# Performance work log

Measured on AMD Instinct MI355X. Metric: run time of the kernel, lower is better.

## Reference

```python
import jax, jax.numpy as jnp
import numpy as np

DIM = 320
D_STATE = 32
D_CONV = 4
EXPAND = 2
HEADDIM = 80
D_INNER = EXPAND * DIM          # 640
NHEADS = D_INNER // HEADDIM     # 8
NGROUPS = 1
CONV_DIM = D_INNER + 2 * NGROUPS * D_STATE          # 704
D_IN_PROJ = 2 * D_INNER + 2 * NGROUPS * D_STATE + NHEADS  # 1352
PATCH = (16, 16, 16)
NUM_PT_EMB = 2


def setup_inputs() -> dict:
    key = jax.random.key(0)
    ks = jax.random.split(key, 16)
    B, Np = 4, 8
    x = jax.random.normal(ks[0], (B, DIM) + PATCH, dtype=jnp.float32)
    point_coords = jax.random.uniform(ks[1], (B, Np, 3), dtype=jnp.float32) * jnp.asarray(PATCH, jnp.float32)
    point_labels = jax.random.randint(ks[2], (B, Np), 0, 2)
    return {
        "x": x,
        "point_coords": point_coords,
        "ln_w": jnp.ones((DIM,), jnp.float32),
        "ln_b": jnp.zeros((DIM,), jnp.float32),
        "in_proj_w": jax.random.normal(ks[3], (D_IN_PROJ, DIM), jnp.float32) * 0.02,
        "conv_w": jax.random.normal(ks[4], (CONV_DIM, 1, D_CONV), jnp.float32) * 0.2,
        "conv_b": jax.random.normal(ks[5], (CONV_DIM,), jnp.float32) * 0.02,
        "dt_bias": jax.random.uniform(ks[6], (NHEADS,), jnp.float32, 0.0, 0.1),
        "A_log": jnp.log(jax.random.uniform(ks[7], (NHEADS,), jnp.float32, 1.0, 16.0)),
        "Dp": jnp.ones((NHEADS,), jnp.float32),
        "rms_w": jnp.ones((D_INNER,), jnp.float32),
        "out_proj_w": jax.random.normal(ks[8], (DIM, D_INNER), jnp.float32) * 0.02,
        "pe_gauss": jax.random.normal(ks[9], (3, DIM // 2), jnp.float32),
        "point_embed": jax.random.normal(ks[10], (NUM_PT_EMB, DIM), jnp.float32) * 0.02,
        "not_a_point": jax.random.normal(ks[11], (DIM,), jnp.float32) * 0.02,
        "point_labels": point_labels,
    }


def _forward(x, point_coords, ln_w, ln_b, in_proj_w, conv_w, conv_b, dt_bias,
             A_log, Dp, rms_w, out_proj_w, pe_gauss, point_embed, not_a_point,
             point_labels):
    B, C = x.shape[:2]
    img_dims = x.shape[2:]
    n_tokens = int(np.prod(img_dims))
    xf = x.reshape(B, C, n_tokens).transpose(0, 2, 1)  # (B, T, C)

    # ---- PointEncoder (SAM-style random Fourier positional embedding) ----
    pc = point_coords / jnp.asarray(PATCH, x.dtype)     # normalize to [0,1]
    pc = 2.0 * pc - 1.0
    pe = (2.0 * jnp.pi) * (pc @ pe_gauss)               # (B, Np, DIM/2)
    pemb = jnp.concatenate([jnp.sin(pe), jnp.cos(pe)], axis=-1)  # (B, Np, DIM)
    lbl = point_labels[..., None]
    safe = jnp.clip(point_labels, 0, NUM_PT_EMB - 1)
    pemb = jnp.where(lbl == -1, not_a_point, pemb + point_embed[safe])

    seq = jnp.concatenate([xf, pemb], axis=1)           # (B, L, C)
    L = seq.shape[1]

    # ---- LayerNorm ----
    mu = seq.mean(-1, keepdims=True)
    var = jnp.mean((seq - mu) ** 2, axis=-1, keepdims=True)
    xn = (seq - mu) * jax.lax.rsqrt(var + 1e-5) * ln_w + ln_b

    # ---- Mamba2 ----
    zxbcdt = xn @ in_proj_w.T                            # (B, L, 1352)
    z = zxbcdt[..., :D_INNER]
    xBC = zxbcdt[..., D_INNER:D_INNER + CONV_DIM]
    dt = zxbcdt[..., D_INNER + CONV_DIM:]                # (B, L, H)
    dt = jax.nn.softplus(dt + dt_bias)

    # causal depthwise conv1d over channels
    conv = jax.lax.conv_general_dilated(
        xBC.transpose(0, 2, 1), conv_w, (1,), [(D_CONV - 1, 0)],
        feature_group_count=CONV_DIM,
        dimension_numbers=("NCH", "OIH", "NCH"))
    xBC = jax.nn.silu((conv + conv_b[None, :, None]).transpose(0, 2, 1))

    xs = xBC[..., :D_INNER].reshape(B, L, NHEADS, HEADDIM)
    Bm = xBC[..., D_INNER:D_INNER + D_STATE]             # (B, L, N), ngroups=1
    Cm = xBC[..., D_INNER + D_STATE:]                    # (B, L, N)

    A = -jnp.exp(A_log)                                  # (H,)
    dA = jnp.exp(dt * A)                                 # (B, L, H)

    def step(h, inp):
        dA_t, dt_t, B_t, C_t, x_t = inp
        h = h * dA_t[:, :, None, None] + jnp.einsum('bh,bn,bhp->bhpn', dt_t, B_t, x_t)
        y = jnp.einsum('bhpn,bn->bhp', h, C_t)
        return h, y

    inps = (dA.transpose(1, 0, 2), dt.transpose(1, 0, 2),
            Bm.transpose(1, 0, 2), Cm.transpose(1, 0, 2),
            xs.transpose(1, 0, 2, 3))
    h0 = jnp.zeros((B, NHEADS, HEADDIM, D_STATE), x.dtype)
    _, ys = jax.lax.scan(step, h0, inps)                 # (L, B, H, P)
    y = ys.transpose(1, 0, 2, 3) + xs * Dp[None, None, :, None]
    y = y.reshape(B, L, D_INNER)

    # gated RMSNorm
    y = y * jax.nn.silu(z)
    y = y * jax.lax.rsqrt(jnp.mean(y * y, axis=-1, keepdims=True) + 1e-5) * rms_w
    out = y @ out_proj_w.T                               # (B, L, DIM)

    out = out[:, :n_tokens].transpose(0, 2, 1).reshape(B, C, *img_dims)
    return out


def reference(x, point_coords, ln_w, ln_b, in_proj_w, conv_w, conv_b, dt_bias,
              A_log, Dp, rms_w, out_proj_w, pe_gauss, point_embed, not_a_point,
              point_labels):
    return _forward(x, point_coords, ln_w, ln_b, in_proj_w, conv_w, conv_b,
                    dt_bias, A_log, Dp, rms_w, out_proj_w, pe_gauss,
                    point_embed, not_a_point, point_labels)
```

## Files before the change

### kernel.cpp

```cpp
#include <hip/hip_runtime.h>
#include <math.h>

#define BQ 4
#define LQ 4104
#define NTQ 4096
#define CDIM 320
#define DIP 1352
#define DI 640
#define CONVD 704
#define NH 8
#define HD 80
#define DS 32
#define MQ (BQ*LQ)
#define QC 64
#define NC 65

typedef __attribute__((ext_vector_type(8))) short bf16x8;
typedef __attribute__((ext_vector_type(4))) float f32x4;

__device__ __forceinline__ unsigned short f2bf(float f){
  union { float f; unsigned u; } v; v.f = f;
  unsigned r = v.u + 0x7FFFu + ((v.u >> 16) & 1u);
  return (unsigned short)(r >> 16);
}
__device__ __forceinline__ float bf2f(unsigned short u){
  union { unsigned u; float f; } v; v.u = ((unsigned)u) << 16;
  return v.f;
}
__device__ __forceinline__ float warp_sum(float v){
  #pragma unroll
  for (int o = 32; o; o >>= 1) v += __shfl_xor(v, o);
  return v;
}
__device__ __forceinline__ void gload16(const unsigned short* g, unsigned short* l){
  __builtin_amdgcn_global_load_lds(
      (const __attribute__((address_space(1))) unsigned int*)g,
      (__attribute__((address_space(3))) unsigned int*)l, 16, 0, 0);
}
__device__ __forceinline__ int swz64(int p, int i){
  return p*QC + (i ^ ((p & 7) << 3));
}

__global__ __launch_bounds__(256) void k_prep(
    const float* __restrict__ w1, unsigned short* __restrict__ w1h,
    const float* __restrict__ w2, const float* __restrict__ rsw,
    unsigned short* __restrict__ w2h,
    const float* __restrict__ x, float* __restrict__ muP, float* __restrict__ s2P,
    const float* __restrict__ pcoords, const float* __restrict__ lnw,
    const float* __restrict__ lnb, const float* __restrict__ pgauss,
    const float* __restrict__ pemb_w, const float* __restrict__ nap,
    const int* __restrict__ plabels, unsigned short* __restrict__ xnh)
{
  const int N1 = DIP*CDIM/4;
  const int N2 = CDIM*DI/4;
  const int NBW = (N1 + N2 + 255)/256;
  int bid = blockIdx.x;
  int t = threadIdx.x;

  if (bid < NBW) {
    int i4 = bid*256 + t;
    if (i4 < N1) {
      float4 v = ((const float4*)w1)[i4];
      unsigned short o[4] = {f2bf(v.x), f2bf(v.y), f2bf(v.z), f2bf(v.w)};
      *(uint2*)&w1h[i4*4] = *(const uint2*)o;
    } else if (i4 - N1 < N2) {
      int j = i4 - N1;
      float4 v = ((const float4*)w2)[j];
      float4 wv = *(const float4*)(rsw + (j*4) % DI);
      unsigned short o[4] = {f2bf(v.x*wv.x), f2bf(v.y*wv.y),
                             f2bf(v.z*wv.z), f2bf(v.w*wv.w)};
      *(uint2*)&w2h[j*4] = *(const uint2*)o;
    }
    return;
  }
  bid -= NBW;
  if (bid < 512) {
    int xblk = bid & 15, sl = (bid >> 4) & 7, b = bid >> 7;
    int cs0 = sl * 40;
    int tok = xblk*256 + t;
    const float* xb = x + ((size_t)b*CDIM)*NTQ;
    float s = 0.f, s2 = 0.f;
    #pragma unroll 8
    for (int c = cs0; c < cs0 + 40; c++) {
      float v = xb[(size_t)c*NTQ + tok];
      s += v; s2 = fmaf(v, v, s2);
    }
    muP[((size_t)sl*BQ + b)*NTQ + tok] = s;
    s2P[((size_t)sl*BQ + b)*NTQ + tok] = s2;
    return;
  }
  bid -= 512;
  int j = bid & 7, b = bid >> 3;
  float p0 = pcoords[(b*8+j)*3+0]*(2.0f/16.0f) - 1.0f;
  float p1 = pcoords[(b*8+j)*3+1]*(2.0f/16.0f) - 1.0f;
  float p2 = pcoords[(b*8+j)*3+2]*(2.0f/16.0f) - 1.0f;
  int lab = plabels[b*8+j];
  int safe = lab < 0 ? 0 : (lab > 1 ? 1 : lab);
  float vA, vB = 0.f;
  {
    int cc = t;
    int f = (cc < 160) ? cc : cc - 160;
    float pe = 6.283185307179586f*(p0*pgauss[f] + p1*pgauss[160+f] + p2*pgauss[320+f]);
    float pv = (cc < 160) ? sinf(pe) : cosf(pe);
    vA = (lab == -1) ? nap[cc] : pv + pemb_w[safe*CDIM + cc];
  }
  if (t < 64) {
    int cc = t + 256;
    int f = cc - 160;
    float pe = 6.283185307179586f*(p0*pgauss[f] + p1*pgauss[160+f] + p2*pgauss[320+f]);
    float pv = cosf(pe);
    vB = (lab == -1) ? nap[cc] : pv + pemb_w[safe*CDIM + cc];
  }
  float s  = warp_sum(vA + vB);
  float s2 = warp_sum(vA*vA + vB*vB);
  __shared__ float r1[4], r2[4];
  int w = t >> 6, lane = t & 63;
  if (lane == 0) { r1[w] = s; r2[w] = s2; }
  __syncthreads();
  float ts  = r1[0]+r1[1]+r1[2]+r1[3];
  float ts2 = r2[0]+r2[1]+r2[2]+r2[3];
  float mu   = ts * (1.0f/CDIM);
  float rsig = rsqrtf(ts2*(1.0f/CDIM) - mu*mu + 1e-5f);
  size_t base = ((size_t)b*LQ + NTQ + j)*CDIM;
  xnh[base + t] = f2bf((vA - mu)*rsig*lnw[t] + lnb[t]);
  if (t < 64)
    xnh[base + t + 256] = f2bf((vB - mu)*rsig*lnw[t+256] + lnb[t+256]);
}

__global__ __launch_bounds__(256) void k_norm_t(
    const float* __restrict__ x, const float* __restrict__ muP,
    const float* __restrict__ s2P, const float* __restrict__ lnw,
    const float* __restrict__ lnb, unsigned short* __restrict__ xnh)
{
  int b = blockIdx.z;
  int c0 = blockIdx.y * 64;
  int t0 = blockIdx.x * 64;
  int t = threadIdx.x;
  int lt = t & 63, cg = t >> 6;
  const float* xb = x + ((size_t)b*CDIM)*NTQ;

  __shared__ unsigned short T[64][72];
  __shared__ float muL[64], rsL[64];
  if (t < 64) {
    float s = 0.f, s2 = 0.f;
    #pragma unroll
    for (int sl = 0; sl < 8; sl++) {
      s  += muP[((size_t)sl*BQ + b)*NTQ + t0 + t];
      s2 += s2P[((size_t)sl*BQ + b)*NTQ + t0 + t];
    }
    float mu = s*(1.0f/CDIM);
    muL[t] = mu;
    rsL[t] = rsqrtf(s2*(1.0f/CDIM) - mu*mu + 1e-5f);
  }
  __syncthreads();
  float mu = muL[lt], rs = rsL[lt];
  #pragma unroll
  for (int c = cg; c < 64; c += 4) {
    float v = xb[(size_t)(c0+c)*NTQ + t0 + lt];
    T[lt][c] = f2bf((v - mu)*rs*lnw[c0+c] + lnb[c0+c]);
  }
  __syncthreads();
  #pragma unroll
  for (int i = 0; i < 4; i++) {
    int idx = t + 256*i;
    int tok = idx >> 4, cq = idx & 15;
    *(uint2*)&xnh[((size_t)(b*LQ) + t0 + tok)*CDIM + c0 + cq*4] =
        *(const uint2*)&T[tok][cq*4];
  }
}

__global__ __launch_bounds__(256) void k_gemm1_mfma(
    const unsigned short* __restrict__ Abf, const unsigned short* __restrict__ Wbf,
    unsigned short* __restrict__ zxh, float* __restrict__ dtraw)
{
  __shared__ unsigned short As[2][128*32];
  __shared__ unsigned short Bs[2][128*32];
  int id = blockIdx.x;
  int xcd = id & 7, pos = id >> 3;
  const int q = 177, r = 3;
  int swz = (xcd < r ? xcd*(q+1) : r*(q+1) + (xcd-r)*q) + pos;
  int m0 = (swz / 11) * 128;
  int n0 = (swz % 11) * 128;
  int tid = threadIdx.x;
  int lane = tid & 63, wid = tid >> 6;
  int wr = wid >> 1, wc = wid & 1;
  int fr = lane & 15, fq = lane >> 4;
  int srow = lane >> 2;
  int scol = (lane & 3) * 8;

#define G1_STAGE(buf, kk)                                                   \
  {                                                                         \
    _Pragma("unroll")                                                       \
    for (int i = 0; i < 2; i++) {                                           \
      int seg = wid + i*4;                                                  \
      int rowA = seg*16 + srow;                                             \
      int ga = m0 + rowA; if (ga > MQ-1) ga = MQ-1;                         \
      gload16(Abf + (size_t)ga*CDIM + (kk) + scol, &As[buf][seg*512]);      \
      int gb = n0 + rowA; if (gb > DIP-1) gb = DIP-1;                       \
      gload16(Wbf + (size_t)gb*CDIM + (kk) + scol, &Bs[buf][seg*512]);      \
    }                                                                       \
  }

#define G1_COMPUTE(buf)                                                     \
  {                                                                         \
    bf16x8 fa[4], fb[4];                                                    \
    _Pragma("unroll")                                                       \
    for (int i = 0; i < 4; i++) {                                           \
      fa[i] = *(const bf16x8*)&As[buf][(wr*64 + i*16 + fr)*32 + fq*8];      \
      fb[i] = *(const bf16x8*)&Bs[buf][(wc*64 + i*16 + fr)*32 + fq*8];      \
    }                                                                       \
    _Pragma("unroll")                                                       \
    for (int i = 0; i < 4; i++)                                             \
      _Pragma("unroll")                                                     \
      for (int j = 0; j < 4; j++)                                           \
        acc[i][j] = __builtin_amdgcn_mfma_f32_16x16x32_bf16(fa[i], fb[j], acc[i][j], 0, 0, 0); \
  }

  f32x4 acc[4][4] = {};
  G1_STAGE(0, 0);
  __syncthreads();
  int cur = 0;
  for (int k0 = 32; k0 < CDIM; k0 += 32) {
    G1_STAGE(cur^1, k0);
    G1_COMPUTE(cur);
    __syncthreads();
    cur ^= 1;
  }
  G1_COMPUTE(cur);

  #pragma unroll
  for (int i = 0; i < 4; i++) {
    #pragma unroll
    for (int j = 0; j < 4; j++) {
      #pragma unroll
      for (int rr = 0; rr < 4; rr++) {
        int grow = m0 + wr*64 + i*16 + fq*4 + rr;
        int gcol = n0 + wc*64 + j*16 + fr;
        if (grow < MQ && gcol < DIP) {
          float v = acc[i][j][rr];
          zxh[(size_t)grow*DIP + gcol] = f2bf(v);
          if (gcol >= DI + CONVD)
            dtraw[(size_t)grow*NH + (gcol - (DI + CONVD))] = v;
        }
      }
    }
  }
}

__global__ __launch_bounds__(256) void k_conv(
    const unsigned short* __restrict__ zxh, const float* __restrict__ cw,
    const float* __restrict__ cb, unsigned short* __restrict__ xcb)
{
  const int nC4 = CONVD/4;
  int gid = blockIdx.x*256 + threadIdx.x;
  if (gid >= (MQ/8)*nC4) return;
  int c4 = gid % nC4;
  int mb = gid / nC4;
  int m0 = mb*8;
  int l0 = m0 % LQ;
  int c0 = c4*4;
  float4 cbv = *(const float4*)(cb + c0);
  float4 w0 = *(const float4*)(cw + (c0+0)*4);
  float4 w1 = *(const float4*)(cw + (c0+1)*4);
  float4 w2 = *(const float4*)(cw + (c0+2)*4);
  float4 w3 = *(const float4*)(cw + (c0+3)*4);
  const float* wp[4] = {(const float*)&w0, (const float*)&w1,
                        (const float*)&w2, (const float*)&w3};
  float vals[11][4];
  #pragma unroll
  for (int r = 0; r < 11; r++) {
    int ls = l0 - 3 + r;
    uint2 u = make_uint2(0,0);
    if (ls >= 0)
      u = *(const uint2*)(zxh + (size_t)(m0-3+r)*DIP + DI + c0);
    vals[r][0] = bf2f((unsigned short)(u.x & 0xffff));
    vals[r][1] = bf2f((unsigned short)(u.x >> 16));
    vals[r][2] = bf2f((unsigned short)(u.y & 0xffff));
    vals[r][3] = bf2f((unsigned short)(u.y >> 16));
  }
  const float* cbp = (const float*)&cbv;
  #pragma unroll
  for (int u = 0; u < 8; u++) {
    unsigned short o[4];
    #pragma unroll
    for (int ch = 0; ch < 4; ch++) {
      float a = cbp[ch];
      #pragma unroll
      for (int j = 0; j < 4; j++)
        a = fmaf(vals[u+j][ch], wp[ch][j], a);
      o[ch] = f2bf(a / (1.f + __expf(-a)));
    }
    *(uint2*)(xcb + (size_t)(m0+u)*CONVD + c0) = *(const uint2*)o;
  }
}

__global__ __launch_bounds__(256) void k_cumsum_state(
    const float* __restrict__ dtraw, const float* __restrict__ dt_bias,
    const float* __restrict__ A_log, const unsigned short* __restrict__ xcb,
    float* __restrict__ dtb, float* __restrict__ cs, float* __restrict__ Dc,
    float* __restrict__ Sbuf)
{
  int c = blockIdx.x, h = blockIdx.y, b = blockIdx.z;
  int len = LQ - c*QC; if (len > QC) len = QC;
  int t = threadIdx.x;
  int lane = t & 63, wid = t >> 6;
  int fr = lane & 15, fq = lane >> 4;
  int m0 = b*LQ + c*QC;

  __shared__ unsigned short XT[HD*QC];
  __shared__ unsigned short BwT[DS*QC];
  __shared__ float ws[QC];

  for (int idx = t; idx < (HD/8)*QC; idx += 256) {
    int pg = idx % 10, i = idx / 10;
    uint4 v = make_uint4(0,0,0,0);
    if (i < len)
      v = *(const uint4*)(xcb + (size_t)(m0+i)*CONVD + h*HD + pg*8);
    union { uint4 u; unsigned short us[8]; } cv; cv.u = v;
    #pragma unroll
    for (int e = 0; e < 8; e++)
      XT[swz64(pg*8+e, i)] = cv.us[e];
  }

  if (t < QC) {
    float A = -expf(A_log[h]);
    float sp = 0.f;
    if (t < len) {
      float v = dtraw[((size_t)(m0+t))*NH + h] + dt_bias[h];
      sp = (v > 20.f) ? v : log1pf(expf(v));
      dtb[((size_t)(m0+t))*NH + h] = sp;
    }
    float a = sp * A;
    #pragma unroll
    for (int off = 1; off < 64; off <<= 1) {
      float pv = __shfl_up(a, off, 64);
      if (t >= off) a += pv;
    }
    cs[((size_t)(b*NH+h)*NC + c)*QC + t] = a;
    if (t == len-1) Dc[(b*NH+h)*NC + c] = expf(a);
    float aEnd = __shfl(a, len-1, 64);
    ws[t] = (t < len) ? __expf(aEnd - a) * sp : 0.f;
  }
  __syncthreads();
  for (int idx = t; idx < DS*QC; idx += 256) {
    int n = idx & 31, i = idx >> 5;
    float v = (i < len) ? bf2f(xcb[(size_t)(m0+i)*CONVD + DI + n]) * ws[i] : 0.f;
    BwT[swz64(n, i)] = f2bf(v);
  }
  __syncthreads();

  size_t base = ((size_t)(b*NC + c)*NH + h)*(HD*DS);
  for (int tp = wid; tp < 10; tp += 4) {
    int pi = tp >> 1, ni = tp & 1;
    f32x4 acc = {};
    #pragma unroll
    for (int ks = 0; ks < 2; ks++) {
      bf16x8 fa = *(const bf16x8*)&XT[swz64(pi*16 + fr, ks*32 + fq*8)];
      bf16x8 fb = *(const bf16x8*)&BwT[swz64(ni*16 + fr, ks*32 + fq*8)];
      acc = __builtin_amdgcn_mfma_f32_16x16x32_bf16(fa, fb, acc, 0, 0, 0);
    }
    #pragma unroll
    for (int rr = 0; rr < 4; rr++)
      Sbuf[base + (size_t)(pi*16 + fq*4 + rr)*DS + ni*16 + fr] = acc[rr];
  }
}

__global__ __launch_bounds__(256) void k_state_scan(
    const float* __restrict__ Sbuf, const float* __restrict__ Dc,
    unsigned short* __restrict__ H0h)
{
  int tid = blockIdx.x*256 + threadIdx.x;
  int pn = tid % (HD*DS);
  int bh = tid / (HD*DS);
  int b = bh >> 3, h = bh & 7;
  float hst = 0.f;
  for (int c = 0; c < NC; c++) {
    size_t idx = ((size_t)(b*NC + c)*NH + h)*(HD*DS) + pn;
    float sv = Sbuf[idx];
    H0h[idx] = f2bf(hst);
    hst = hst * Dc[bh*NC + c] + sv;
  }
}

__global__ __launch_bounds__(256) void k_chunk_y_mfma(
    const unsigned short* __restrict__ xcb, const unsigned short* __restrict__ zxh,
    const float* __restrict__ dtb, const float* __restrict__ cs,
    const unsigned short* __restrict__ H0h, const float* __restrict__ Dp,
    unsigned short* __restrict__ ygb, float* __restrict__ ssum8)
{
  int c = blockIdx.x, h = blockIdx.y, b = blockIdx.z;
  int len = LQ - c*QC; if (len > QC) len = QC;
  int t = threadIdx.x;
  int lane = t & 63, wid = t >> 6;
  int fr = lane & 15, fq = lane >> 4;
  int m0 = b*LQ + c*QC;

  __shared__ unsigned short XT[HD*QC];
  __shared__ unsigned short Wt[4*16*32];
  __shared__ float slA[QC], dtlA[QC], elA[QC];

  const float* csb = cs + ((size_t)(b*NH+h)*NC + c)*QC;

  for (int idx = t; idx < (HD/8)*QC; idx += 256) {
    int pg = idx % 10, i = idx / 10;
    uint4 v = make_uint4(0,0,0,0);
    if (i < len)
      v = *(const uint4*)(xcb + (size_t)(m0+i)*CONVD + h*HD + pg*8);
    union { uint4 u; unsigned short us[8]; } cv; cv.u = v;
    #pragma unroll
    for (int e = 0; e < 8; e++)
      XT[swz64(pg*8+e, i)] = cv.us[e];
  }
  if (t < QC) {
    float s = csb[t];
    slA[t] = s;
    elA[t] = __expf(s);
    dtlA[t] = (t < len) ? dtb[((size_t)(m0+t))*NH + h] : 0.f;
  }
  __syncthreads();

  int row16 = wid*16 + fr;
  bf16x8 fa = {};
  if (row16 < len)
    fa = *(const bf16x8*)(xcb + (size_t)(m0+row16)*CONVD + DI + DS + fq*8);

  size_t hb = ((size_t)(b*NC + c)*NH + h)*(HD*DS);
  f32x4 acc[5];
  #pragma unroll
  for (int j = 0; j < 5; j++) {
    int p = j*16 + fr;
    bf16x8 fb = *(const bf16x8*)(H0h + hb + (size_t)p*DS + fq*8);
    f32x4 z = {};
    acc[j] = __builtin_amdgcn_mfma_f32_16x16x32_bf16(fa, fb, z, 0, 0, 0);
  }
  #pragma unroll
  for (int rr = 0; rr < 4; rr++) {
    float el = elA[wid*16 + fq*4 + rr];
    #pragma unroll
    for (int j = 0; j < 5; j++) acc[j][rr] *= el;
  }

  int wbase = wid << 9;
  for (int sc = 0; sc < 2; sc++) {
    int i0 = sc*32;
    #pragma unroll
    for (int jt = 0; jt < 2; jt++) {
      int col = i0 + jt*16 + fr;
      bf16x8 fbv = {};
      if (col < len)
        fbv = *(const bf16x8*)(xcb + (size_t)(m0+col)*CONVD + DI + fq*8);
      float sc_col = slA[col], dt_col = dtlA[col];
      f32x4 z = {};
      f32x4 g = __builtin_amdgcn_mfma_f32_16x16x32_bf16(fa, fbv, z, 0, 0, 0);
      #pragma unroll
      for (int rr = 0; rr < 4; rr++) {
        int lr = fq*4 + rr;
        int row = wid*16 + lr;
        float v = 0.f;
        if (col <= row)
          v = g[rr] * __expf(slA[row] - sc_col) * dt_col;
        int lc = jt*16 + fr;
        int slot = (lc >> 3) ^ (lr & 3);
        Wt[wbase + (lr<<5) + (slot<<3) + (lc&7)] = f2bf(v);
      }
    }
    bf16x8 wa = *(const bf16x8*)&Wt[wbase + (fr<<5) + ((fq ^ (fr&3))<<3)];
    #pragma unroll
    for (int j = 0; j < 5; j++) {
      int p = j*16 + fr;
      bf16x8 xb = *(const bf16x8*)&XT[swz64(p, i0 + fq*8)];
      acc[j] = __builtin_amdgcn_mfma_f32_16x16x32_bf16(wa, xb, acc[j], 0, 0, 0);
    }
  }

  float dpv = Dp[h];
  #pragma unroll
  for (int rr = 0; rr < 4; rr++) {
    int l = wid*16 + fq*4 + rr;
    if (l >= len) continue;
    size_t m = m0 + l;
    float ssp = 0.f;
    #pragma unroll
    for (int j = 0; j < 5; j++) {
      int p = j*16 + fr;
      int cc = h*HD + p;
      float xv = bf2f(XT[swz64(p, l)]);
      float y = acc[j][rr] + xv*dpv;
      float zv = bf2f(zxh[m*DIP + cc]);
      y *= zv / (1.f + __expf(-zv));
      ygb[m*DI + cc] = f2bf(y);
      ssp = fmaf(y, y, ssp);
    }
    #pragma unroll
    for (int o = 1; o < 16; o <<= 1) ssp += __shfl_xor(ssp, o);
    if (fr == 0) ssum8[m*NH + h] = ssp;
  }
}

__global__ __launch_bounds__(256) void k_gemm2_mfma(
    const unsigned short* __restrict__ W2h, const unsigned short* __restrict__ Ygh,
    const float* __restrict__ ssum8, float* __restrict__ out)
{
  __shared__ unsigned short As[2][128*32];
  __shared__ unsigned short Bs[2][128*32];
  int id = blockIdx.x;
  int xcd = id & 7, pos = id >> 3;
  const int q = 48, r = 3;
  int swz = (xcd < r ? xcd*(q+1) : r*(q+1) + (xcd-r)*q) + pos;
  int c0 = (swz % 3) * 128;
  int t0 = (swz / 3) * 128;
  int tid = threadIdx.x;
  int lane = tid & 63, wid = tid >> 6;
  int wr = wid >> 1, wc = wid & 1;
  int fr = lane & 15, fq = lane >> 4;
  int srow = lane >> 2;
  int scol = (lane & 3) * 8;

#define G2_STAGE(buf, kk)                                                   \
  {                                                                         \
    _Pragma("unroll")                                                       \
    for (int i = 0; i < 2; i++) {                                           \
      int seg = wid + i*4;                                                  \
      int rowA = seg*16 + srow;                                             \
      int ga = c0 + rowA; if (ga > CDIM-1) ga = CDIM-1;                     \
      gload16(W2h + (size_t)ga*DI + (kk) + scol, &As[buf][seg*512]);        \
      int gb = t0 + rowA; if (gb > MQ-1) gb = MQ-1;                         \
      gload16(Ygh + (size_t)gb*DI + (kk) + scol, &Bs[buf][seg*512]);        \
    }                                                                       \
  }

#define G2_COMPUTE(buf)                                                     \
  {                                                                         \
    bf16x8 fa[4], fb[4];                                                    \
    _Pragma("unroll")                                                       \
    for (int i = 0; i < 4; i++) {                                           \
      fa[i] = *(const bf16x8*)&As[buf][(wr*64 + i*16 + fr)*32 + fq*8];      \
      fb[i] = *(const bf16x8*)&Bs[buf][(wc*64 + i*16 + fr)*32 + fq*8];      \
    }                                                                       \
    _Pragma("unroll")                                                       \
    for (int i = 0; i < 4; i++)                                             \
      _Pragma("unroll")                                                     \
      for (int j = 0; j < 4; j++)                                           \
        acc[i][j] = __builtin_amdgcn_mfma_f32_16x16x32_bf16(fa[i], fb[j], acc[i][j], 0, 0, 0); \
  }

  f32x4 acc[4][4] = {};
  G2_STAGE(0, 0);
  __syncthreads();
  int cur = 0;
  for (int k0 = 32; k0 < DI; k0 += 32) {
    G2_STAGE(cur^1, k0);
    G2_COMPUTE(cur);
    __syncthreads();
    cur ^= 1;
  }
  G2_COMPUTE(cur);

  float rsvj[4];
  #pragma unroll
  for (int j = 0; j < 4; j++) {
    int tok = t0 + wc*64 + j*16 + fr;
    float ss = 0.f;
    if (tok < MQ) {
      float4 a = *(const float4*)(ssum8 + (size_t)tok*NH);
      float4 bb = *(const float4*)(ssum8 + (size_t)tok*NH + 4);
      ss = (a.x + a.y + a.z + a.w) + (bb.x + bb.y + bb.z + bb.w);
    }
    rsvj[j] = rsqrtf(ss*(1.0f/DI) + 1e-5f);
  }

  #pragma unroll
  for (int i = 0; i < 4; i++) {
    #pragma unroll
    for (int j = 0; j < 4; j++) {
      #pragma unroll
      for (int rr = 0; rr < 4; rr++) {
        int ch  = c0 + wr*64 + i*16 + fq*4 + rr;
        int tok = t0 + wc*64 + j*16 + fr;
        if (ch < CDIM && tok < MQ) {
          int b = tok / LQ, l = tok % LQ;
          if (l < NTQ)
            out[((size_t)(b*CDIM + ch))*NTQ + l] = acc[i][j][rr] * rsvj[j];
        }
      }
    }
  }
}

extern "C" void kernel_launch(void* const* d_in, const int* in_sizes, int n_in,
                              void* d_out, int out_size, void* d_ws, size_t ws_size,
                              hipStream_t stream)
{
  const float* x       = (const float*)d_in[0];
  const float* pc      = (const float*)d_in[1];
  const float* lnw     = (const float*)d_in[2];
  const float* lnb     = (const float*)d_in[3];
  const float* w1      = (const float*)d_in[4];
  const float* cw      = (const float*)d_in[5];
  const float* cb      = (const float*)d_in[6];
  const float* dt_bias = (const float*)d_in[7];
  const float* A_log   = (const float*)d_in[8];
  const float* Dp      = (const float*)d_in[9];
  const float* rsw     = (const float*)d_in[10];
  const float* w2      = (const float*)d_in[11];
  const float* pg      = (const float*)d_in[12];
  const float* pew     = (const float*)d_in[13];
  const float* nap     = (const float*)d_in[14];
  const int*   plab    = (const int*)d_in[15];
  float* out = (float*)d_out;

  unsigned short* xnh  = (unsigned short*)d_ws;
  unsigned short* zxh  = xnh + (size_t)MQ*CDIM;
  float* dtraw = (float*)(zxh + (size_t)MQ*DIP);
  unsigned short* xcb  = (unsigned short*)(dtraw + (size_t)MQ*NH);
  float* dtb = (float*)(xcb + (size_t)MQ*CONVD);
  float* cs  = dtb + (size_t)MQ*NH;
  float* Dc  = cs  + (size_t)BQ*NH*NC*QC;
  float* Sb  = Dc  + (size_t)BQ*NH*NC;
  unsigned short* H0h = (unsigned short*)(Sb + (size_t)BQ*NC*NH*HD*DS);
  unsigned short* ygb = H0h + (size_t)BQ*NC*NH*HD*DS;
  unsigned short* w1h = ygb + (size_t)MQ*DI;
  unsigned short* w2h = w1h + (size_t)DIP*CDIM;
  float* muP = (float*)(w2h + (size_t)CDIM*DI);
  float* s2P = muP + (size_t)8*BQ*NTQ;
  float* ssum8 = s2P + (size_t)8*BQ*NTQ;

  const int NBW = (DIP*CDIM/4 + CDIM*DI/4 + 255)/256;
  k_prep<<<NBW + 512 + 32, 256, 0, stream>>>(
      w1, w1h, w2, rsw, w2h, x, muP, s2P,
      pc, lnw, lnb, pg, pew, nap, plab, xnh);
  dim3 gn(NTQ/64, CDIM/64, BQ);
  k_norm_t<<<gn, 256, 0, stream>>>(x, muP, s2P, lnw, lnb, xnh);
  k_gemm1_mfma<<<129*11, 256, 0, stream>>>(xnh, w1h, zxh, dtraw);
  k_conv<<<((MQ/8)*(CONVD/4) + 255)/256, 256, 0, stream>>>(zxh, cw, cb, xcb);
  dim3 gc(NC, NH, BQ);
  k_cumsum_state<<<gc, 256, 0, stream>>>(dtraw, dt_bias, A_log, xcb, dtb, cs, Dc, Sb);
  k_state_scan<<<(BQ*NH*HD*DS)/256, 256, 0, stream>>>(Sb, Dc, H0h);
  k_chunk_y_mfma<<<gc, 256, 0, stream>>>(xcb, zxh, dtb, cs, H0h, Dp, ygb, ssum8);
  k_gemm2_mfma<<<129*3, 256, 0, stream>>>(w2h, ygb, ssum8, out);
}
```

Measured before the change: 149.7 us.

## Fuse LayerNorm stats into single pass, fold conv into cumsum kernel, stage GEMM1 output via LDS

LayerNorm now runs in one kernel that reads each x column once, keeps a bf16 copy in LDS and computes mean and variance in place, replacing the separate partial-sum pass. The standalone depthwise conv+SiLU kernel is removed: the cumsum/state kernel computes the conv for its own head's x channels and for the B/C channels (written by head 0), which saves a launch and the xcb reload. GEMM1 writes its bf16 output through a swizzled LDS tile so global stores are 16-byte and coalesced. The trade-offs are redundant conv work on the B channels across heads, scalar zxh loads for B/C, and one-pass LayerNorm statistics computed from raw sums with bf16-staged values.

```diff
diff --git a/kernel.cpp b/kernel.cpp
--- a/kernel.cpp
+++ b/kernel.cpp
@@ -45,7 +45,6 @@
     const float* __restrict__ w1, unsigned short* __restrict__ w1h,
     const float* __restrict__ w2, const float* __restrict__ rsw,
     unsigned short* __restrict__ w2h,
-    const float* __restrict__ x, float* __restrict__ muP, float* __restrict__ s2P,
     const float* __restrict__ pcoords, const float* __restrict__ lnw,
     const float* __restrict__ lnb, const float* __restrict__ pgauss,
     const float* __restrict__ pemb_w, const float* __restrict__ nap,
@@ -74,22 +73,6 @@
     return;
   }
   bid -= NBW;
-  if (bid < 512) {
-    int xblk = bid & 15, sl = (bid >> 4) & 7, b = bid >> 7;
-    int cs0 = sl * 40;
-    int tok = xblk*256 + t;
-    const float* xb = x + ((size_t)b*CDIM)*NTQ;
-    float s = 0.f, s2 = 0.f;
-    #pragma unroll 8
-    for (int c = cs0; c < cs0 + 40; c++) {
-      float v = xb[(size_t)c*NTQ + tok];
-      s += v; s2 = fmaf(v, v, s2);
-    }
-    muP[((size_t)sl*BQ + b)*NTQ + tok] = s;
-    s2P[((size_t)sl*BQ + b)*NTQ + tok] = s2;
-    return;
-  }
-  bid -= 512;
   int j = bid & 7, b = bid >> 3;
   float p0 = pcoords[(b*8+j)*3+0]*(2.0f/16.0f) - 1.0f;
   float p1 = pcoords[(b*8+j)*3+1]*(2.0f/16.0f) - 1.0f;
@@ -127,45 +110,51 @@
     xnh[base + t + 256] = f2bf((vB - mu)*rsig*lnw[t+256] + lnb[t+256]);
 }
 
-__global__ __launch_bounds__(256) void k_norm_t(
-    const float* __restrict__ x, const float* __restrict__ muP,
-    const float* __restrict__ s2P, const float* __restrict__ lnw,
+__global__ __launch_bounds__(256) void k_ln(
+    const float* __restrict__ x, const float* __restrict__ lnw,
     const float* __restrict__ lnb, unsigned short* __restrict__ xnh)
 {
-  int b = blockIdx.z;
-  int c0 = blockIdx.y * 64;
-  int t0 = blockIdx.x * 64;
+  int b = blockIdx.y;
+  int t0 = blockIdx.x * 32;
   int t = threadIdx.x;
-  int lt = t & 63, cg = t >> 6;
+  int lt = t & 31, cg = t >> 5;
   const float* xb = x + ((size_t)b*CDIM)*NTQ;
 
-  __shared__ unsigned short T[64][72];
-  __shared__ float muL[64], rsL[64];
-  if (t < 64) {
-    float s = 0.f, s2 = 0.f;
-    #pragma unroll
-    for (int sl = 0; sl < 8; sl++) {
-      s  += muP[((size_t)sl*BQ + b)*NTQ + t0 + t];
-      s2 += s2P[((size_t)sl*BQ + b)*NTQ + t0 + t];
-    }
-    float mu = s*(1.0f/CDIM);
+  __shared__ unsigned short XC[CDIM][33];
+  __shared__ float sA[8][32], s2A[8][32];
+  __shared__ float muL[32], rsL[32];
+
+  float s = 0.f, s2 = 0.f;
+  for (int c = cg; c < CDIM; c += 8) {
+    float v = xb[(size_t)c*NTQ + t0 + lt];
+    s += v; s2 = fmaf(v, v, s2);
+    XC[c][lt] = f2bf(v);
+  }
+  sA[cg][lt] = s; s2A[cg][lt] = s2;
+  __syncthreads();
+  if (t < 32) {
+    float ts = 0.f, ts2 = 0.f;
+    #pragma unroll
+    for (int g = 0; g < 8; g++) { ts += sA[g][t]; ts2 += s2A[g][t]; }
+    float mu = ts*(1.0f/CDIM);
     muL[t] = mu;
-    rsL[t] = rsqrtf(s2*(1.0f/CDIM) - mu*mu + 1e-5f);
-  }
-  __syncthreads();
-  float mu = muL[lt], rs = rsL[lt];
-  #pragma unroll
-  for (int c = cg; c < 64; c += 4) {
-    float v = xb[(size_t)(c0+c)*NTQ + t0 + lt];
-    T[lt][c] = f2bf((v - mu)*rs*lnw[c0+c] + lnb[c0+c]);
-  }
-  __syncthreads();
-  #pragma unroll
-  for (int i = 0; i < 4; i++) {
-    int idx = t + 256*i;
-    int tok = idx >> 4, cq = idx & 15;
-    *(uint2*)&xnh[((size_t)(b*LQ) + t0 + tok)*CDIM + c0 + cq*4] =
-        *(const uint2*)&T[tok][cq*4];
+    rsL[t] = rsqrtf(ts2*(1.0f/CDIM) - mu*mu + 1e-5f);
+  }
+  __syncthreads();
+  #pragma unroll
+  for (int it = 0; it < 10; it++) {
+    int idx = t + it*256;
+    int tok = idx / 80, g4 = idx % 80;
+    int c0 = g4*4;
+    float mu = muL[tok], rs = rsL[tok];
+    float4 wv = *(const float4*)(lnw + c0);
+    float4 bv = *(const float4*)(lnb + c0);
+    unsigned short o[4];
+    o[0] = f2bf((bf2f(XC[c0+0][tok]) - mu)*rs*wv.x + bv.x);
+    o[1] = f2bf((bf2f(XC[c0+1][tok]) - mu)*rs*wv.y + bv.y);
+    o[2] = f2bf((bf2f(XC[c0+2][tok]) - mu)*rs*wv.z + bv.z);
+    o[3] = f2bf((bf2f(XC[c0+3][tok]) - mu)*rs*wv.w + bv.w);
+    *(uint2*)&xnh[((size_t)(b*LQ) + t0 + tok)*CDIM + c0] = *(const uint2*)o;
   }
 }
 
@@ -173,8 +162,9 @@
     const unsigned short* __restrict__ Abf, const unsigned short* __restrict__ Wbf,
     unsigned short* __restrict__ zxh, float* __restrict__ dtraw)
 {
-  __shared__ unsigned short As[2][128*32];
-  __shared__ unsigned short Bs[2][128*32];
+  __shared__ unsigned short SM[16384];
+#define AS1(buf) (SM + (buf)*4096)
+#define BS1(buf) (SM + 8192 + (buf)*4096)
   int id = blockIdx.x;
   int xcd = id & 7, pos = id >> 3;
   const int q = 177, r = 3;
@@ -195,9 +185,9 @@
       int seg = wid + i*4;                                                  \
       int rowA = seg*16 + srow;                                             \
       int ga = m0 + rowA; if (ga > MQ-1) ga = MQ-1;                         \
-      gload16(Abf + (size_t)ga*CDIM + (kk) + scol, &As[buf][seg*512]);      \
+      gload16(Abf + (size_t)ga*CDIM + (kk) + scol, AS1(buf) + seg*512);     \
       int gb = n0 + rowA; if (gb > DIP-1) gb = DIP-1;                       \
-      gload16(Wbf + (size_t)gb*CDIM + (kk) + scol, &Bs[buf][seg*512]);      \
+      gload16(Wbf + (size_t)gb*CDIM + (kk) + scol, BS1(buf) + seg*512);     \
     }                                                                       \
   }
 
@@ -206,8 +196,8 @@
     bf16x8 fa[4], fb[4];                                                    \
     _Pragma("unroll")                                                       \
     for (int i = 0; i < 4; i++) {                                           \
-      fa[i] = *(const bf16x8*)&As[buf][(wr*64 + i*16 + fr)*32 + fq*8];      \
-      fb[i] = *(const bf16x8*)&Bs[buf][(wc*64 + i*16 + fr)*32 + fq*8];      \
+      fa[i] = *(const bf16x8*)(AS1(buf) + (wr*64 + i*16 + fr)*32 + fq*8);   \
+      fb[i] = *(const bf16x8*)(BS1(buf) + (wc*64 + i*16 + fr)*32 + fq*8);   \
     }                                                                       \
     _Pragma("unroll")                                                       \
     for (int i = 0; i < 4; i++)                                             \
@@ -227,6 +217,7 @@
     cur ^= 1;
   }
   G1_COMPUTE(cur);
+  __syncthreads();
 
   #pragma unroll
   for (int i = 0; i < 4; i++) {
@@ -234,71 +225,38 @@
     for (int j = 0; j < 4; j++) {
       #pragma unroll
       for (int rr = 0; rr < 4; rr++) {
-        int grow = m0 + wr*64 + i*16 + fq*4 + rr;
-        int gcol = n0 + wc*64 + j*16 + fr;
-        if (grow < MQ && gcol < DIP) {
-          float v = acc[i][j][rr];
-          zxh[(size_t)grow*DIP + gcol] = f2bf(v);
-          if (gcol >= DI + CONVD)
-            dtraw[(size_t)grow*NH + (gcol - (DI + CONVD))] = v;
-        }
+        int rowL = wr*64 + i*16 + fq*4 + rr;
+        int colL = wc*64 + j*16 + fr;
+        float v = acc[i][j][rr];
+        int gcol = n0 + colL;
+        if (gcol >= DI + CONVD && m0 + rowL < MQ)
+          dtraw[(size_t)(m0+rowL)*NH + (gcol - (DI + CONVD))] = v;
+        int g = colL >> 3;
+        int gs = (g + 2*fq) & 15;
+        SM[rowL*128 + gs*8 + (colL & 7)] = f2bf(v);
       }
     }
   }
-}
-
-__global__ __launch_bounds__(256) void k_conv(
-    const unsigned short* __restrict__ zxh, const float* __restrict__ cw,
-    const float* __restrict__ cb, unsigned short* __restrict__ xcb)
-{
-  const int nC4 = CONVD/4;
-  int gid = blockIdx.x*256 + threadIdx.x;
-  if (gid >= (MQ/8)*nC4) return;
-  int c4 = gid % nC4;
-  int mb = gid / nC4;
-  int m0 = mb*8;
-  int l0 = m0 % LQ;
-  int c0 = c4*4;
-  float4 cbv = *(const float4*)(cb + c0);
-  float4 w0 = *(const float4*)(cw + (c0+0)*4);
-  float4 w1 = *(const float4*)(cw + (c0+1)*4);
-  float4 w2 = *(const float4*)(cw + (c0+2)*4);
-  float4 w3 = *(const float4*)(cw + (c0+3)*4);
-  const float* wp[4] = {(const float*)&w0, (const float*)&w1,
-                        (const float*)&w2, (const float*)&w3};
-  float vals[11][4];
-  #pragma unroll
-  for (int r = 0; r < 11; r++) {
-    int ls = l0 - 3 + r;
-    uint2 u = make_uint2(0,0);
-    if (ls >= 0)
-      u = *(const uint2*)(zxh + (size_t)(m0-3+r)*DIP + DI + c0);
-    vals[r][0] = bf2f((unsigned short)(u.x & 0xffff));
-    vals[r][1] = bf2f((unsigned short)(u.x >> 16));
-    vals[r][2] = bf2f((unsigned short)(u.y & 0xffff));
-    vals[r][3] = bf2f((unsigned short)(u.y >> 16));
-  }
-  const float* cbp = (const float*)&cbv;
-  #pragma unroll
-  for (int u = 0; u < 8; u++) {
-    unsigned short o[4];
-    #pragma unroll
-    for (int ch = 0; ch < 4; ch++) {
-      float a = cbp[ch];
-      #pragma unroll
-      for (int j = 0; j < 4; j++)
-        a = fmaf(vals[u+j][ch], wp[ch][j], a);
-      o[ch] = f2bf(a / (1.f + __expf(-a)));
-    }
-    *(uint2*)(xcb + (size_t)(m0+u)*CONVD + c0) = *(const uint2*)o;
+  __syncthreads();
+  int rows = MQ - m0; if (rows > 128) rows = 128;
+  int cols = DIP - n0; if (cols > 128) cols = 128;
+  #pragma unroll
+  for (int it = 0; it < 8; it++) {
+    int idx = tid + it*256;
+    int row = idx >> 4, g = idx & 15;
+    int fqr = (row >> 2) & 3;
+    int gs = (g + 2*fqr) & 15;
+    if (row < rows && g*8 < cols)
+      *(uint4*)&zxh[(size_t)(m0+row)*DIP + n0 + g*8] = *(const uint4*)&SM[row*128 + gs*8];
   }
 }
 
 __global__ __launch_bounds__(256) void k_cumsum_state(
     const float* __restrict__ dtraw, const float* __restrict__ dt_bias,
-    const float* __restrict__ A_log, const unsigned short* __restrict__ xcb,
-    float* __restrict__ dtb, float* __restrict__ cs, float* __restrict__ Dc,
-    float* __restrict__ Sbuf)
+    const float* __restrict__ A_log, const unsigned short* __restrict__ zxh,
+    const float* __restrict__ cw, const float* __restrict__ cb,
+    unsigned short* __restrict__ xcb, float* __restrict__ dtb,
+    float* __restrict__ cs, float* __restrict__ Dc, float* __restrict__ Sbuf)
 {
   int c = blockIdx.x, h = blockIdx.y, b = blockIdx.z;
   int len = LQ - c*QC; if (len > QC) len = QC;
@@ -313,13 +271,53 @@
 
   for (int idx = t; idx < (HD/8)*QC; idx += 256) {
     int pg = idx % 10, i = idx / 10;
-    uint4 v = make_uint4(0,0,0,0);
-    if (i < len)
-      v = *(const uint4*)(xcb + (size_t)(m0+i)*CONVD + h*HD + pg*8);
-    union { uint4 u; unsigned short us[8]; } cv; cv.u = v;
+    int l = c*QC + i;
+    unsigned short o[8] = {0,0,0,0,0,0,0,0};
+    if (i < len) {
+      int ch0 = h*HD + pg*8;
+      float a[8];
+      #pragma unroll
+      for (int e = 0; e < 8; e++) a[e] = cb[ch0+e];
+      #pragma unroll
+      for (int j = 0; j < 4; j++) {
+        int ls = l - 3 + j;
+        if (ls >= 0) {
+          uint4 u = *(const uint4*)(zxh + (size_t)(b*LQ+ls)*DIP + DI + ch0);
+          union { uint4 u; unsigned short us[8]; } cv; cv.u = u;
+          #pragma unroll
+          for (int e = 0; e < 8; e++)
+            a[e] = fmaf(bf2f(cv.us[e]), cw[(ch0+e)*4 + j], a[e]);
+        }
+      }
+      #pragma unroll
+      for (int e = 0; e < 8; e++)
+        o[e] = f2bf(a[e] / (1.f + __expf(-a[e])));
+      *(uint4*)&xcb[(size_t)(m0+i)*CONVD + ch0] = *(const uint4*)o;
+    }
     #pragma unroll
     for (int e = 0; e < 8; e++)
-      XT[swz64(pg*8+e, i)] = cv.us[e];
+      XT[swz64(pg*8+e, i)] = o[e];
+  }
+
+  for (int idx = t; idx < 2*DS*QC; idx += 256) {
+    int which = idx >> 11;
+    if (which == 1 && h != 0) continue;
+    int r2 = idx & 2047; int n = r2 & 31, i = r2 >> 5;
+    int l = c*QC + i;
+    unsigned short ob = 0;
+    if (i < len) {
+      int chx = DI + which*DS + n;
+      float a = cb[chx];
+      #pragma unroll
+      for (int j = 0; j < 4; j++) {
+        int ls = l - 3 + j;
+        if (ls >= 0)
+          a = fmaf(bf2f(zxh[(size_t)(b*LQ+ls)*DIP + DI + chx]), cw[chx*4 + j], a);
+      }
+      ob = f2bf(a / (1.f + __expf(-a)));
+      if (h == 0) xcb[(size_t)(m0+i)*CONVD + chx] = ob;
+    }
+    if (which == 0) BwT[swz64(n, i)] = ob;
   }
 
   if (t < QC) {
@@ -342,10 +340,11 @@
     ws[t] = (t < len) ? __expf(aEnd - a) * sp : 0.f;
   }
   __syncthreads();
+
   for (int idx = t; idx < DS*QC; idx += 256) {
     int n = idx & 31, i = idx >> 5;
-    float v = (i < len) ? bf2f(xcb[(size_t)(m0+i)*CONVD + DI + n]) * ws[i] : 0.f;
-    BwT[swz64(n, i)] = f2bf(v);
+    int a = swz64(n, i);
+    BwT[a] = f2bf(bf2f(BwT[a]) * ws[i]);
   }
   __syncthreads();
 
@@ -621,20 +620,18 @@
   unsigned short* ygb = H0h + (size_t)BQ*NC*NH*HD*DS;
   unsigned short* w1h = ygb + (size_t)MQ*DI;
   unsigned short* w2h = w1h + (size_t)DIP*CDIM;
-  float* muP = (float*)(w2h + (size_t)CDIM*DI);
-  float* s2P = muP + (size_t)8*BQ*NTQ;
-  float* ssum8 = s2P + (size_t)8*BQ*NTQ;
+  float* ssum8 = (float*)(w2h + (size_t)CDIM*DI);
 
   const int NBW = (DIP*CDIM/4 + CDIM*DI/4 + 255)/256;
-  k_prep<<<NBW + 512 + 32, 256, 0, stream>>>(
-      w1, w1h, w2, rsw, w2h, x, muP, s2P,
+  k_prep<<<NBW + 32, 256, 0, stream>>>(
+      w1, w1h, w2, rsw, w2h,
       pc, lnw, lnb, pg, pew, nap, plab, xnh);
-  dim3 gn(NTQ/64, CDIM/64, BQ);
-  k_norm_t<<<gn, 256, 0, stream>>>(x, muP, s2P, lnw, lnb, xnh);
+  dim3 gl(NTQ/32, BQ);
+  k_ln<<<gl, 256, 0, stream>>>(x, lnw, lnb, xnh);
   k_gemm1_mfma<<<129*11, 256, 0, stream>>>(xnh, w1h, zxh, dtraw);
-  k_conv<<<((MQ/8)*(CONVD/4) + 255)/256, 256, 0, stream>>>(zxh, cw, cb, xcb);
   dim3 gc(NC, NH, BQ);
-  k_cumsum_state<<<gc, 256, 0, stream>>>(dtraw, dt_bias, A_log, xcb, dtb, cs, Dc, Sb);
+  k_cumsum_state<<<gc, 256, 0, stream>>>(dtraw, dt_bias, A_log, zxh, cw, cb,
+                                         xcb, dtb, cs, Dc, Sb);
   k_state_scan<<<(BQ*NH*HD*DS)/256, 256, 0, stream>>>(Sb, Dc, H0h);
   k_chunk_y_mfma<<<gc, 256, 0, stream>>>(xcb, zxh, dtb, cs, H0h, Dp, ygb, ssum8);
   k_gemm2_mfma<<<129*3, 256, 0, stream>>>(w2h, ygb, ssum8, out);
```

New measurement: 236.6 us. +58.1%, slower.
